# Kernel optimization log

Measured on AMD Instinct MI355X. Metric: run time of the kernel, lower is better.

The kernel has to match this reference:

```python
import jax, jax.numpy as jnp
import numpy as np

NUM_CLASSES = 50000
FEATURE_DIM = 512
BATCH = 4096
NUM_INTERNAL = NUM_CLASSES - 1
TREE_DEPTH = int(np.ceil(np.log2(NUM_CLASSES)))  # 16


def _build_path_maps():
    # Replicates the __init__ loop: for each class leaf, walk to root.
    path_nodes = np.full((NUM_CLASSES, TREE_DEPTH), -1, dtype=np.int32)
    path_dirs = np.full((NUM_CLASSES, TREE_DEPTH), -1, dtype=np.int32)
    for c in range(NUM_CLASSES):
        curr = NUM_INTERNAL + c
        nodes, dirs = [], []
        while curr > 0:
            parent = (curr - 1) // 2
            nodes.append(parent)
            dirs.append((curr - 1) % 2)
            curr = parent
        L = len(nodes)
        path_nodes[c, :L] = nodes[::-1]
        path_dirs[c, :L] = dirs[::-1]
    return jnp.asarray(path_nodes), jnp.asarray(path_dirs)


def setup_inputs() -> dict:
    key = jax.random.key(0)
    k1, k2, k3 = jax.random.split(key, 3)
    features = jax.random.normal(k1, (BATCH, FEATURE_DIM), dtype=jnp.float32)
    targets = jax.random.randint(k2, (BATCH, 1), 0, NUM_CLASSES, dtype=jnp.int32)
    # glorot_uniform over (NUM_INTERNAL, FEATURE_DIM, 2): fan_in=FEATURE_DIM, fan_out=2
    limit = float(np.sqrt(6.0 / (FEATURE_DIM + 2)))
    node_weights = jax.random.uniform(k3, (NUM_INTERNAL, FEATURE_DIM, 2),
                                      minval=-limit, maxval=limit, dtype=jnp.float32)
    path_nodes_map, path_directions_map = _build_path_maps()
    return {"features": features, "targets": targets, "node_weights": node_weights,
            "path_nodes_map": path_nodes_map, "path_directions_map": path_directions_map}


def reference(features, targets, node_weights, path_nodes_map, path_directions_map):
    targets_flat = jnp.squeeze(targets.astype(jnp.int32), axis=-1)          # [B]
    batch_path_nodes = jnp.take(path_nodes_map, targets_flat, axis=0)       # [B, K]
    batch_path_dirs = jnp.take(path_directions_map, targets_flat, axis=0)   # [B, K]
    mask = (batch_path_nodes != -1).astype(features.dtype)                  # [B, K]
    safe_nodes = jnp.where(batch_path_nodes == -1, 0, batch_path_nodes)
    path_weights = jnp.take(node_weights, safe_nodes, axis=0)               # [B, K, D, 2]
    node_logits = jnp.einsum('bd,bkdc->bkc', features, path_weights)        # [B, K, 2]
    node_log_probs = jax.nn.log_softmax(node_logits, axis=-1)               # [B, K, 2]
    safe_dirs = jnp.where(batch_path_dirs == -1, 0, batch_path_dirs)
    selected = jnp.take_along_axis(node_log_probs, safe_dirs[..., None], axis=-1)[..., 0]
    total_log_prob = jnp.sum(selected * mask, axis=-1)                      # [B]
    return -total_log_prob
```

## Files before the change

kernel.cpp:

```cpp
#include <hip/hip_runtime.h>
#include <math.h>


constexpr int BATCH = 4096;
constexpr int FDIM  = 512;
constexpr int DEPTH = 16;

__global__ __launch_bounds__(256) void hstree_loss(
    const float* __restrict__ features,
    const int*   __restrict__ targets,
    const float* __restrict__ node_weights,
    const int*   __restrict__ path_nodes,
    const int*   __restrict__ path_dirs,
    float*       __restrict__ out)
{
    const int lane = threadIdx.x & 63;
    const int b    = (blockIdx.x << 2) + (threadIdx.x >> 6);
    if (b >= BATCH) return;

    const int t = __builtin_amdgcn_readfirstlane(targets[b]);

    int nodes[DEPTH];
    int dirs[DEPTH];
#pragma unroll
    for (int k = 0; k < DEPTH; ++k) {
        nodes[k] = path_nodes[t * DEPTH + k];
        dirs[k]  = path_dirs [t * DEPTH + k];
    }

    const float4* fb = (const float4*)(features + (size_t)b * FDIM);
    const float4 f0 = fb[lane];
    const float4 f1 = fb[lane + 64];

    auto wbase = [&](int k) -> const float4* {
        int n = nodes[k] < 0 ? 0 : nodes[k];
        return (const float4*)(node_weights + (size_t)n * (FDIM * 2));
    };

    const float4* wp = wbase(0);
    float4 a0 = wp[2 * lane];
    float4 a1 = wp[2 * lane + 1];
    float4 a2 = wp[128 + 2 * lane];
    float4 a3 = wp[128 + 2 * lane + 1];

    float loss = 0.0f;

#pragma unroll 1
    for (int k = 0; k < DEPTH; ++k) {
        const int kn = (k + 1 < DEPTH) ? (k + 1) : k;
        const float4* np = wbase(kn);
        float4 b0 = np[2 * lane];
        float4 b1 = np[2 * lane + 1];
        float4 b2 = np[128 + 2 * lane];
        float4 b3 = np[128 + 2 * lane + 1];

        float l0 = f0.x * a0.x + f0.y * a0.z + f0.z * a1.x + f0.w * a1.z
                 + f1.x * a2.x + f1.y * a2.z + f1.z * a3.x + f1.w * a3.z;
        float l1 = f0.x * a0.y + f0.y * a0.w + f0.z * a1.y + f0.w * a1.w
                 + f1.x * a2.y + f1.y * a2.w + f1.z * a3.y + f1.w * a3.w;

#pragma unroll
        for (int off = 32; off; off >>= 1) {
            l0 += __shfl_xor(l0, off, 64);
            l1 += __shfl_xor(l1, off, 64);
        }

        if (nodes[k] >= 0) {
            const float z = (dirs[k] == 0) ? (l0 - l1) : (l1 - l0);
            loss += fmaxf(-z, 0.0f) + log1pf(__expf(-fabsf(z)));
        }

        a0 = b0; a1 = b1; a2 = b2; a3 = b3;
    }

    if (lane == 0) out[b] = loss;
}

extern "C" void kernel_launch(void* const* d_in, const int* in_sizes, int n_in,
                              void* d_out, int out_size, void* d_ws, size_t ws_size,
                              hipStream_t stream) {
    const float* features     = (const float*)d_in[0];
    const int*   targets      = (const int*)  d_in[1];
    const float* node_weights = (const float*)d_in[2];
    const int*   path_nodes   = (const int*)  d_in[3];
    const int*   path_dirs    = (const int*)  d_in[4];
    float*       out          = (float*)d_out;

    hstree_loss<<<BATCH / 4, 256, 0, stream>>>(
        features, targets, node_weights, path_nodes, path_dirs, out);
}
```

Measured before the change: 265.2 us.

## Deepen weight prefetch to four nodes and batch the logit-difference reductions

Replaces the one-step double buffer with a four-deep ring of weight loads, so more independent gathers are in flight per wave. The two logits are collapsed into a single difference dot product before reduction, which halves the shuffle work, and all 16 reductions are batched after the loop. The loop is fully unrolled, log1pf becomes __logf(1+x), and an occupancy hint of four blocks per CU is set. This raises register use and slightly lowers precision in the softplus term.

```diff
diff --git a/kernel.cpp b/kernel.cpp
--- a/kernel.cpp
+++ b/kernel.cpp
@@ -6,7 +6,7 @@
 constexpr int FDIM  = 512;
 constexpr int DEPTH = 16;
 
-__global__ __launch_bounds__(256) void hstree_loss(
+__global__ __launch_bounds__(256, 4) void hstree_loss(
     const float* __restrict__ features,
     const int*   __restrict__ targets,
     const float* __restrict__ node_weights,
@@ -16,7 +16,6 @@
 {
     const int lane = threadIdx.x & 63;
     const int b    = (blockIdx.x << 2) + (threadIdx.x >> 6);
-    if (b >= BATCH) return;
 
     const int t = __builtin_amdgcn_readfirstlane(targets[b]);
 
@@ -32,45 +31,54 @@
     const float4 f0 = fb[lane];
     const float4 f1 = fb[lane + 64];
 
-    auto wbase = [&](int k) -> const float4* {
-        int n = nodes[k] < 0 ? 0 : nodes[k];
+    auto wptr = [&](int k) -> const float4* {
+        const int n = nodes[k] < 0 ? 0 : nodes[k];
         return (const float4*)(node_weights + (size_t)n * (FDIM * 2));
     };
 
-    const float4* wp = wbase(0);
-    float4 a0 = wp[2 * lane];
-    float4 a1 = wp[2 * lane + 1];
-    float4 a2 = wp[128 + 2 * lane];
-    float4 a3 = wp[128 + 2 * lane + 1];
+    const int o0 = 2 * lane;
+    const int o1 = 2 * lane + 1;
+    const int o2 = 128 + 2 * lane;
+    const int o3 = 129 + 2 * lane;
+
+    float4 buf[4][4];
+#pragma unroll
+    for (int k = 0; k < 4; ++k) {
+        const float4* p = wptr(k);
+        buf[k][0] = p[o0]; buf[k][1] = p[o1];
+        buf[k][2] = p[o2]; buf[k][3] = p[o3];
+    }
+
+    float zp[DEPTH];
+#pragma unroll
+    for (int k = 0; k < DEPTH; ++k) {
+        const float4 a0 = buf[k & 3][0], a1 = buf[k & 3][1];
+        const float4 a2 = buf[k & 3][2], a3 = buf[k & 3][3];
+        if (k + 4 < DEPTH) {
+            const float4* p = wptr(k + 4);
+            buf[k & 3][0] = p[o0]; buf[k & 3][1] = p[o1];
+            buf[k & 3][2] = p[o2]; buf[k & 3][3] = p[o3];
+        }
+        zp[k] = f0.x * (a0.x - a0.y) + f0.y * (a0.z - a0.w)
+              + f0.z * (a1.x - a1.y) + f0.w * (a1.z - a1.w)
+              + f1.x * (a2.x - a2.y) + f1.y * (a2.z - a2.w)
+              + f1.z * (a3.x - a3.y) + f1.w * (a3.z - a3.w);
+    }
+
+#pragma unroll
+    for (int k = 0; k < DEPTH; ++k) {
+#pragma unroll
+        for (int off = 32; off; off >>= 1)
+            zp[k] += __shfl_xor(zp[k], off, 64);
+    }
 
     float loss = 0.0f;
-
-#pragma unroll 1
+#pragma unroll
     for (int k = 0; k < DEPTH; ++k) {
-        const int kn = (k + 1 < DEPTH) ? (k + 1) : k;
-        const float4* np = wbase(kn);
-        float4 b0 = np[2 * lane];
-        float4 b1 = np[2 * lane + 1];
-        float4 b2 = np[128 + 2 * lane];
-        float4 b3 = np[128 + 2 * lane + 1];
-
-        float l0 = f0.x * a0.x + f0.y * a0.z + f0.z * a1.x + f0.w * a1.z
-                 + f1.x * a2.x + f1.y * a2.z + f1.z * a3.x + f1.w * a3.z;
-        float l1 = f0.x * a0.y + f0.y * a0.w + f0.z * a1.y + f0.w * a1.w
-                 + f1.x * a2.y + f1.y * a2.w + f1.z * a3.y + f1.w * a3.w;
-
-#pragma unroll
-        for (int off = 32; off; off >>= 1) {
-            l0 += __shfl_xor(l0, off, 64);
-            l1 += __shfl_xor(l1, off, 64);
+        if (nodes[k] >= 0) {
+            const float s = (dirs[k] == 0) ? zp[k] : -zp[k];
+            loss += fmaxf(-s, 0.0f) + __logf(1.0f + __expf(-fabsf(s)));
         }
-
-        if (nodes[k] >= 0) {
-            const float z = (dirs[k] == 0) ? (l0 - l1) : (l1 - l0);
-            loss += fmaxf(-z, 0.0f) + log1pf(__expf(-fabsf(z)));
-        }
-
-        a0 = b0; a1 = b1; a2 = b2; a3 = b3;
     }
 
     if (lane == 0) out[b] = loss;
```

Result: no change. 267.0 us (+0.6%).
